# Performance work log

Hardware: AMD Instinct MI355X
Metric: run time of the kernel (lower is better)

## Reference

```python
import jax, jax.numpy as jnp
import numpy as np

D_MODEL, D_STATE, D_CONV, EXPAND = 1024, 16, 4, 2
D_INNER = EXPAND * D_MODEL          # 2048
DT_RANK = -(-D_MODEL // 16)        # 64
B_SZ, SEQ = 4, 2048


def setup_inputs() -> dict:
    key = jax.random.key(0)
    ks = jax.random.split(key, 10)
    s = 0.02
    x = jax.random.normal(ks[0], (B_SZ, SEQ, D_MODEL), jnp.float32)
    in_proj_w = s * jax.random.normal(ks[1], (2, 2 * D_INNER, D_MODEL), jnp.float32)
    conv_w = s * jax.random.normal(ks[2], (2, D_INNER, D_CONV), jnp.float32)
    conv_b = s * jax.random.normal(ks[3], (2, D_INNER), jnp.float32)
    x_proj_w = s * jax.random.normal(ks[4], (2, DT_RANK + 2 * D_STATE, D_INNER), jnp.float32)
    dt_proj_w = s * jax.random.normal(ks[5], (2, D_INNER, DT_RANK), jnp.float32)
    # bias chosen so softplus(dt) is small and the scan is stable (mamba-style dt init)
    dt_proj_b = jax.random.uniform(ks[6], (2, D_INNER), jnp.float32, -5.0, -3.0)
    # A_log = log(A) with A in [1, d_state], per real Mamba init (S4D-real)
    A_log = jnp.log(jax.random.uniform(ks[7], (2, D_INNER, D_STATE), jnp.float32, 1.0, float(D_STATE)))
    D_param = jnp.ones((2, D_INNER), jnp.float32) + s * jax.random.normal(ks[8], (2, D_INNER), jnp.float32)
    out_proj_w = s * jax.random.normal(ks[9], (2, D_MODEL, D_INNER), jnp.float32)
    return {"x": x, "in_proj_w": in_proj_w, "conv_w": conv_w, "conv_b": conv_b,
            "x_proj_w": x_proj_w, "dt_proj_w": dt_proj_w, "dt_proj_b": dt_proj_b,
            "A_log": A_log, "D_param": D_param, "out_proj_w": out_proj_w}


def _mamba(x, in_w, cw, cb, xw, dtw, dtb, A_log, Dp, ow):
    """Single-direction Mamba forward. x: [B, L, d_model]."""
    B, L, _ = x.shape
    xz = jnp.einsum('bld,ed->ble', x, in_w)          # [B, L, 2*d_inner]
    xi, z = jnp.split(xz, 2, axis=-1)
    # depthwise causal conv1d over time, kernel d_conv
    xp = jnp.pad(xi, ((0, 0), (D_CONV - 1, 0), (0, 0)))
    xc = cb + sum(cw[:, k] * xp[:, k:k + L, :] for k in range(D_CONV))
    xc = jax.nn.silu(xc)                              # [B, L, d_inner]
    proj = jnp.einsum('bld,ed->ble', xc, xw)          # [B, L, dt_rank+2*d_state]
    dt_raw, Bm, Cm = jnp.split(proj, [DT_RANK, DT_RANK + D_STATE], axis=-1)
    dt = jax.nn.softplus(jnp.einsum('blr,dr->bld', dt_raw, dtw) + dtb)  # [B, L, d_inner]
    A = -jnp.exp(A_log)                               # [d_inner, d_state]

    def step(h, inp):
        dt_t, B_t, C_t, x_t = inp                     # [B,d_inner],[B,S],[B,S],[B,d_inner]
        dA = jnp.exp(dt_t[..., None] * A)             # [B, d_inner, d_state]
        h = h * dA + (dt_t * x_t)[..., None] * B_t[:, None, :]
        y = jnp.einsum('bds,bs->bd', h, C_t)
        return h, y

    h0 = jnp.zeros((B, D_INNER, D_STATE), x.dtype)
    inps = (dt.transpose(1, 0, 2), Bm.transpose(1, 0, 2),
            Cm.transpose(1, 0, 2), xc.transpose(1, 0, 2))
    _, ys = jax.lax.scan(step, h0, inps)              # ys: [L, B, d_inner]
    y = ys.transpose(1, 0, 2) + xc * Dp
    y = y * jax.nn.silu(z)
    return jnp.einsum('bld,md->blm', y, ow)           # [B, L, d_model]


def reference(x, in_proj_w, conv_w, conv_b, x_proj_w, dt_proj_w, dt_proj_b, A_log, D_param, out_proj_w):
    y_f = _mamba(x, in_proj_w[0], conv_w[0], conv_b[0], x_proj_w[0],
                 dt_proj_w[0], dt_proj_b[0], A_log[0], D_param[0], out_proj_w[0])
    xb = jnp.flip(x, axis=1)
    y_b = _mamba(xb, in_proj_w[1], conv_w[1], conv_b[1], x_proj_w[1],
                 dt_proj_w[1], dt_proj_b[1], A_log[1], D_param[1], out_proj_w[1])
    return y_f + jnp.flip(y_b, axis=1)
```

## Files before the change

kernel.cpp:

```cpp
#include <hip/hip_runtime.h>
#include <hip/hip_bf16.h>
#include <math.h>
#include <stdio.h>


using u16 = unsigned short;
using u32 = unsigned int;

typedef __bf16 bf16x8 __attribute__((ext_vector_type(8)));
typedef float  f32x4  __attribute__((ext_vector_type(4)));
typedef u32    u32x4  __attribute__((ext_vector_type(4)));
typedef u16    u16x4  __attribute__((ext_vector_type(4)));

#define DEVINL __device__ __forceinline__

DEVINL float b2f(u16 u) { union { u32 i; float f; } v; v.i = ((u32)u) << 16; return v.f; }
DEVINL u16 f2b(float f) {
  union { float f; u32 i; } v; v.f = f;
  u32 i = v.i;
  return (u16)((i + 0x7FFFu + ((i >> 16) & 1u)) >> 16);
}

#define L2E 1.4426950408889634f
#define LN2 0.6931471805599453f

DEVINL float fast_silu(float a) {
  const float e = __builtin_amdgcn_exp2f(-a * L2E);
  return a * __builtin_amdgcn_rcpf(1.f + e);
}
DEVINL float fast_softplus(float x) {
  if (x > 20.f) return x;
  return LN2 * __builtin_amdgcn_logf(1.f + __builtin_amdgcn_exp2f(x * L2E));
}

DEVINL void gl_lds16(const u16* g, u16* l) {
  __builtin_amdgcn_global_load_lds(
      (__attribute__((address_space(1))) void*)const_cast<u16*>(g),
      (__attribute__((address_space(3))) void*)l, 16, 0, 0);
}

#define BAR()   asm volatile("s_barrier" ::: "memory")
#define LGKM0() asm volatile("s_waitcnt lgkmcnt(0)" ::: "memory")
#define VM6()   asm volatile("s_waitcnt vmcnt(6)" ::: "memory")
#define VM0()   asm volatile("s_waitcnt vmcnt(0)" ::: "memory")
#define NOPS    ((void)0)

__global__ __launch_bounds__(512, 2) void k_gemm256(
    const u16* __restrict__ A, int lda, int flipA,
    const u16* __restrict__ Bw, int ldb,
    u16* __restrict__ C, int ldc, int K)
{
  extern __shared__ __align__(16) char lds[];

  const int tid  = threadIdx.x;
  const int lane = tid & 63;
  const int wid  = tid >> 6;

  const int mBase = blockIdx.x * 256;
  const int nBase = blockIdx.y * 256;

  const int rloc = lane >> 3;
  const int scol = ((lane & 7) ^ rloc) << 3;
  const u16* srcA[2][2];
  const u16* srcB[2][2];
#pragma unroll
  for (int h = 0; h < 2; ++h)
#pragma unroll
    for (int i = 0; i < 2; ++i) {
      int ra = mBase + h * 128 + wid * 16 + i * 8 + rloc;
      if (flipA) ra ^= 2047;
      const int rb = nBase + h * 128 + wid * 16 + i * 8 + rloc;
      srcA[h][i] = A  + (long long)ra * lda + scol;
      srcB[h][i] = Bw + (long long)rb * ldb + scol;
    }
  u16* const dA = (u16*)lds + wid * 1024;
  u16* const dB = (u16*)lds + 32768 + wid * 1024;

  const int lhi16 = (lane >> 4) * 16;
  const int swz   = (lane & 7) << 4;
  const int rdA   = ((wid >> 2) * 64 + (lane & 15)) * 128 + (lhi16 ^ swz);
  const int rdAx  = rdA ^ 64;
  const int rdB   = 65536 + ((wid & 3) * 32 + (lane & 15)) * 128 + (lhi16 ^ swz);
  const int rdBx  = rdB ^ 64;

  f32x4 acc[2][2][4][2];
#pragma unroll
  for (int a = 0; a < 2; ++a)
#pragma unroll
    for (int b = 0; b < 2; ++b)
#pragma unroll
      for (int c = 0; c < 4; ++c)
#pragma unroll
        for (int d = 0; d < 2; ++d) acc[a][b][c][d] = (f32x4){0.f, 0.f, 0.f, 0.f};

  bf16x8 af[4][2], bq0[2][2], bq1[2][2];

#define LDSV(off) (*(const bf16x8*)(lds + (off)))
#define READ_A(CB, QM) do {                                                    \
  _Pragma("unroll") for (int fm = 0; fm < 4; ++fm) {                           \
    af[fm][0] = LDSV((CB)*32768 + (QM)*16384 + fm*2048 + rdA);                 \
    af[fm][1] = LDSV((CB)*32768 + (QM)*16384 + fm*2048 + rdAx); }              \
} while (0)
#define READ_B(CB, QN, DST) do {                                               \
  _Pragma("unroll") for (int fn = 0; fn < 2; ++fn) {                           \
    DST[fn][0] = LDSV((CB)*32768 + (QN)*16384 + fn*2048 + rdB);                \
    DST[fn][1] = LDSV((CB)*32768 + (QN)*16384 + fn*2048 + rdBx); }             \
} while (0)
#define MMA(QM, QN, BFR) do {                                                  \
  __builtin_amdgcn_s_setprio(1);                                              \
  _Pragma("unroll") for (int fm = 0; fm < 4; ++fm)                             \
  _Pragma("unroll") for (int fn = 0; fn < 2; ++fn)                             \
  _Pragma("unroll") for (int kk = 0; kk < 2; ++kk)                             \
    acc[QM][QN][fm][fn] = __builtin_amdgcn_mfma_f32_16x16x32_bf16(             \
        af[fm][kk], BFR[fn][kk], acc[QM][QN][fm][fn], 0, 0, 0);                \
  __builtin_amdgcn_s_setprio(0);                                              \
} while (0)
#define STAGE_A(CB, H, KT) do {                                                \
  gl_lds16(srcA[H][0] + (KT)*64, dA + (CB)*16384 + (H)*8192);                  \
  gl_lds16(srcA[H][1] + (KT)*64, dA + (CB)*16384 + (H)*8192 + 512);            \
} while (0)
#define STAGE_B(CB, H, KT) do {                                                \
  gl_lds16(srcB[H][0] + (KT)*64, dB + (CB)*16384 + (H)*8192);                  \
  gl_lds16(srcB[H][1] + (KT)*64, dB + (CB)*16384 + (H)*8192 + 512);            \
} while (0)

#define KTILE(CB, S1, S2, S3, S4, VMW) do {                                    \
  READ_A(CB, 0); READ_B(CB, 0, bq0);                                           \
  S1;                                                                          \
  LGKM0(); MMA(0, 0, bq0); BAR();                                              \
  READ_B(CB, 1, bq1);                                                          \
  S2;                                                                          \
  LGKM0(); MMA(0, 1, bq1); BAR();                                              \
  READ_A(CB, 1);                                                               \
  S3;                                                                          \
  LGKM0(); MMA(1, 1, bq1); BAR();                                              \
  S4; VMW;                                                                     \
  MMA(1, 0, bq0); BAR();                                                       \
} while (0)

  STAGE_A(0, 0, 0); STAGE_B(0, 0, 0); STAGE_A(0, 1, 0); STAGE_B(0, 1, 0);
  STAGE_A(1, 0, 1); STAGE_B(1, 1, 1); STAGE_A(1, 1, 1);
  VM6();
  BAR();

  const int niter = K >> 7;
  for (int it = 0; it < niter - 1; ++it) {
    const int kt = 2 * it;
    KTILE(0,
          STAGE_B(1, 0, kt + 1),
          STAGE_A(0, 0, kt + 2),
          STAGE_B(0, 1, kt + 2),
          STAGE_A(0, 1, kt + 2),
          VM6());
    KTILE(1,
          STAGE_B(0, 0, kt + 2),
          STAGE_A(1, 0, kt + 3),
          STAGE_B(1, 1, kt + 3),
          STAGE_A(1, 1, kt + 3),
          VM6());
  }
  {
    const int kt = 2 * (niter - 1);
    KTILE(0, STAGE_B(1, 0, kt + 1), NOPS, NOPS, NOPS, VM0());
    KTILE(1, NOPS, NOPS, NOPS, NOPS, NOPS);
  }

  const int rq = (lane >> 4) << 2;
  const int cn = lane & 15;
  const long long mW = mBase + (wid >> 2) * 64;
  const int nW = nBase + (wid & 3) * 32;
#pragma unroll
  for (int qm = 0; qm < 2; ++qm)
#pragma unroll
    for (int qn = 0; qn < 2; ++qn)
#pragma unroll
      for (int fm = 0; fm < 4; ++fm)
#pragma unroll
        for (int fn = 0; fn < 2; ++fn)
#pragma unroll
          for (int r = 0; r < 4; ++r) {
            const long long m = mW + qm * 128 + fm * 16 + rq + r;
            const int n = nW + qn * 128 + fn * 16 + cn;
            C[m * ldc + n] = f2b(acc[qm][qn][fm][fn][r]);
          }
#undef LDSV
#undef READ_A
#undef READ_B
#undef MMA
#undef STAGE_A
#undef STAGE_B
#undef KTILE
}

template <int MODE>
__global__ __launch_bounds__(256) void k_gemm(
    const u16* __restrict__ A, int lda, int flipA,
    const u16* __restrict__ Bw, int ldb,
    void* __restrict__ Cout, int ldc, int K,
    float* __restrict__ f1, float* __restrict__ f2,
    float* __restrict__ out2)
{
  __shared__ __align__(16) u16 As[128 * 64];
  __shared__ __align__(16) u16 Bs[128 * 64];

  const int tid  = threadIdx.x;
  const int lane = tid & 63;
  const int wid  = tid >> 6;

  const int mBase = blockIdx.x * 128;
  const int nBase = blockIdx.y * 128;

  f32x4 acc[4][4];
#pragma unroll
  for (int i = 0; i < 4; ++i)
#pragma unroll
    for (int j = 0; j < 4; ++j) acc[i][j] = (f32x4){0.f, 0.f, 0.f, 0.f};

  const int wm = (wid & 1) * 64;
  const int wn = (wid >> 1) * 64;
  const int lrow = lane & 15;
  const int lk   = (lane >> 4) * 8;
  const int sr = tid >> 3;
  const int sc = (tid & 7) * 8;

  for (int k0 = 0; k0 < K; k0 += 64) {
#pragma unroll
    for (int i = 0; i < 4; ++i) {
      int ra = mBase + i * 32 + sr;
      if (flipA) ra ^= 2047;
      const int rb = nBase + i * 32 + sr;
      u16* la = &As[(i * 256 + wid * 64) * 8];
      u16* lb = &Bs[(i * 256 + wid * 64) * 8];
      gl_lds16(A  + (long long)ra * lda + (k0 + sc), la);
      gl_lds16(Bw + (long long)rb * ldb + (k0 + sc), lb);
    }
    __syncthreads();
#pragma unroll
    for (int kk = 0; kk < 64; kk += 32) {
      bf16x8 af[4], bfr[4];
#pragma unroll
      for (int f = 0; f < 4; ++f) {
        af[f]  = *(const bf16x8*)&As[(wm + f * 16 + lrow) * 64 + kk + lk];
        bfr[f] = *(const bf16x8*)&Bs[(wn + f * 16 + lrow) * 64 + kk + lk];
      }
#pragma unroll
      for (int fm = 0; fm < 4; ++fm)
#pragma unroll
        for (int fn = 0; fn < 4; ++fn)
          acc[fm][fn] = __builtin_amdgcn_mfma_f32_16x16x32_bf16(af[fm], bfr[fn], acc[fm][fn], 0, 0, 0);
    }
    __syncthreads();
  }

  const int rowq = (lane >> 4) * 4;
  const int coln = lane & 15;
#pragma unroll
  for (int fm = 0; fm < 4; ++fm) {
#pragma unroll
    for (int fn = 0; fn < 4; ++fn) {
#pragma unroll
      for (int r = 0; r < 4; ++r) {
        const long long m = mBase + wm + fm * 16 + rowq + r;
        const long long n = nBase + wn + fn * 16 + coln;
        const float v = acc[fm][fn][r];
        if constexpr (MODE == 0) {
          ((u16*)Cout)[m * ldc + n] = f2b(v);
        } else if constexpr (MODE == 1) {
          ((u16*)Cout)[m * ldc + n] = f2b(fast_softplus(v + f1[(int)n]));
        } else if constexpr (MODE == 2) {
          ((float*)Cout)[m * ldc + n] = v;
        } else if constexpr (MODE == 3) {
          const long long mf = m ^ 2047;
          out2[mf * ldc + n] = v + f2[mf * ldc + n];
        } else {
          if (n < 64)       ((u16*)Cout)[m * ldc + n] = f2b(v);
          else if (n < 80)  f1[m * 16 + (n - 64)] = v;
          else if (n < 96)  f2[m * 16 + (n - 80)] = v;
        }
      }
    }
  }
}

__global__ __launch_bounds__(256) void k_prep(
    const float* __restrict__ inw_d, u16* __restrict__ inwB,
    const float* __restrict__ xpw_d, u16* __restrict__ xw_pad,
    const float* __restrict__ dtw_d, u16* __restrict__ dtwB,
    const float* __restrict__ alog_d, float* __restrict__ A2,
    const float* __restrict__ cw_d, float* __restrict__ cwT)
{
  const int bx = blockIdx.x;
  const int tid = threadIdx.x;
  if (bx < 4096) {
    const int i = bx * 256 + tid;
    const f32x4 v = ((const f32x4*)inw_d)[i];
    u16x4 o = {f2b(v[0]), f2b(v[1]), f2b(v[2]), f2b(v[3])};
    ((u16x4*)inwB)[i] = o;
  } else if (bx < 5120) {
    const int idx = (bx - 4096) * 256 + tid;
    const int c = idx & 2047, r = idx >> 11;
    xw_pad[idx] = (r < 96) ? f2b(xpw_d[r * 2048 + c]) : (u16)0;
  } else if (bx < 5248) {
    const int i = (bx - 5120) * 256 + tid;
    const f32x4 v = ((const f32x4*)dtw_d)[i];
    u16x4 o = {f2b(v[0]), f2b(v[1]), f2b(v[2]), f2b(v[3])};
    ((u16x4*)dtwB)[i] = o;
  } else if (bx < 5376) {
    const int idx = (bx - 5248) * 256 + tid;
    A2[idx] = -expf(alog_d[idx]) * L2E;
  } else {
    const int idx = (bx - 5376) * 256 + tid;
    const int d = idx & 2047, k = idx >> 11;
    cwT[k * 2048 + d] = cw_d[d * 4 + k];
  }
}

__global__ __launch_bounds__(256) void k_castw(const float* __restrict__ src,
                                               u16* __restrict__ dst) {
  const int i = blockIdx.x * 256 + threadIdx.x;
  const f32x4 v = ((const f32x4*)src)[i];
  u16x4 o = {f2b(v[0]), f2b(v[1]), f2b(v[2]), f2b(v[3])};
  ((u16x4*)dst)[i] = o;
}

__global__ __launch_bounds__(256) void k_cast_x(const float* __restrict__ x,
                                                u16* __restrict__ xA) {
  const int idx = blockIdx.x * 256 + threadIdx.x;
  const f32x4 v = ((const f32x4*)x)[idx];
  u16x4 o = {f2b(v[0]), f2b(v[1]), f2b(v[2]), f2b(v[3])};
  ((u16x4*)xA)[idx] = o;
}

__global__ __launch_bounds__(256) void k_conv(const u16* __restrict__ xz,
                                              const float* __restrict__ cwT,
                                              const float* __restrict__ cb,
                                              u16* __restrict__ xc) {
  const int idx = blockIdx.x * 256 + threadIdx.x;
  const int d8  = idx & 255;
  const int gr  = idx >> 8;
  const int t   = gr & 2047;
  const int d0  = d8 * 8;

  float acc[8];
  {
    const f32x4 b0 = *(const f32x4*)(cb + d0);
    const f32x4 b1 = *(const f32x4*)(cb + d0 + 4);
#pragma unroll
    for (int j = 0; j < 4; ++j) { acc[j] = b0[j]; acc[4 + j] = b1[j]; }
  }

#pragma unroll
  for (int k = 0; k < 4; ++k) {
    const int tt = t - 3 + k;
    if (tt < 0) continue;
    const u32x4 v = *(const u32x4*)(xz + (long long)(gr + k - 3) * 4096 + d0);
    const u16* pv = (const u16*)&v;
    const f32x4 w0 = *(const f32x4*)(cwT + k * 2048 + d0);
    const f32x4 w1 = *(const f32x4*)(cwT + k * 2048 + d0 + 4);
#pragma unroll
    for (int j = 0; j < 4; ++j) {
      acc[j]     = fmaf(w0[j], b2f(pv[j]), acc[j]);
      acc[4 + j] = fmaf(w1[j], b2f(pv[4 + j]), acc[4 + j]);
    }
  }
  u16 o[8];
#pragma unroll
  for (int j = 0; j < 8; ++j) {
    o[j] = f2b(fast_silu(acc[j]));
  }
  *(u32x4*)(xc + (long long)gr * 2048 + d0) = *(const u32x4*)o;
}

__global__ __launch_bounds__(256) void k_scanA(
    const u16* __restrict__ dt, const u16* __restrict__ xc,
    const float* __restrict__ Bf, const float* __restrict__ A2,
    float* __restrict__ hbuf, float* __restrict__ sumdt)
{
  const int tid = threadIdx.x;
  const int bx  = blockIdx.x;
  const int d     = (bx & 7) * 256 + tid;
  const int chunk = (bx >> 3) & 31;
  const int b     = bx >> 8;

  float a2[16];
#pragma unroll
  for (int s = 0; s < 16; ++s) a2[s] = A2[d * 16 + s];

  float h[16];
#pragma unroll
  for (int s = 0; s < 16; ++s) h[s] = 0.f;
  float sdt = 0.f;

  const long long rowBase = (long long)b * 2048 + chunk * 64;
  for (int t0 = 0; t0 < 64; ++t0) {
    const long long gr = rowBase + t0;
    const float dtv = b2f(dt[gr * 2048 + d]);
    const float xcv = b2f(xc[gr * 2048 + d]);
    sdt += dtv;
    const float dtx = dtv * xcv;
    float Bv[16];
    *(f32x4*)&Bv[0]  = *(const f32x4*)(Bf + gr * 16);
    *(f32x4*)&Bv[4]  = *(const f32x4*)(Bf + gr * 16 + 4);
    *(f32x4*)&Bv[8]  = *(const f32x4*)(Bf + gr * 16 + 8);
    *(f32x4*)&Bv[12] = *(const f32x4*)(Bf + gr * 16 + 12);
#pragma unroll
    for (int s = 0; s < 16; ++s) {
      const float dA = __builtin_amdgcn_exp2f(a2[s] * dtv);
      h[s] = fmaf(h[s], dA, dtx * Bv[s]);
    }
  }
  const long long cbi = (long long)b * 32 + chunk;
#pragma unroll
  for (int s = 0; s < 16; ++s) hbuf[(cbi * 16 + s) * 2048 + d] = h[s];
  sumdt[cbi * 2048 + d] = sdt;
}

__global__ __launch_bounds__(256) void k_scanB(
    const float* __restrict__ A2, float* __restrict__ hbuf,
    const float* __restrict__ sumdt)
{
  const int tid = threadIdx.x;
  const int bx  = blockIdx.x;
  const int d   = (bx & 7) * 256 + tid;
  const int sg  = ((bx >> 3) & 1) * 8;
  const int b   = bx >> 4;

  float a2[8];
#pragma unroll
  for (int s = 0; s < 8; ++s) a2[s] = A2[d * 16 + sg + s];
  float h[8];
#pragma unroll
  for (int s = 0; s < 8; ++s) h[s] = 0.f;

  const long long base = (long long)b * 32;
  for (int c = 0; c < 32; ++c) {
    const long long cbi = base + c;
    const float sd = sumdt[cbi * 2048 + d];
#pragma unroll
    for (int s = 0; s < 8; ++s) {
      float* p = &hbuf[(cbi * 16 + sg + s) * 2048 + d];
      const float loc = *p;
      *p = h[s];
      const float P = __builtin_amdgcn_exp2f(a2[s] * sd);
      h[s] = fmaf(h[s], P, loc);
    }
  }
}

__global__ __launch_bounds__(256) void k_scanC(
    const u16* __restrict__ dt, const u16* __restrict__ xc,
    const float* __restrict__ Bf, const float* __restrict__ Cf,
    const float* __restrict__ A2, const float* __restrict__ hbuf,
    const float* __restrict__ Dp, u16* __restrict__ yz)
{
  const int tid = threadIdx.x;
  const int bx  = blockIdx.x;
  const int d     = (bx & 7) * 256 + tid;
  const int chunk = (bx >> 3) & 31;
  const int b     = bx >> 8;
  const float dp  = Dp[d];

  float a2[16];
#pragma unroll
  for (int s = 0; s < 16; ++s) a2[s] = A2[d * 16 + s];

  const long long cbi = (long long)b * 32 + chunk;
  float h[16];
#pragma unroll
  for (int s = 0; s < 16; ++s) h[s] = hbuf[(cbi * 16 + s) * 2048 + d];

  const long long rowBase = (long long)b * 2048 + chunk * 64;
  for (int t0 = 0; t0 < 64; ++t0) {
    const long long gr = rowBase + t0;
    const float dtv = b2f(dt[gr * 2048 + d]);
    const float xcv = b2f(xc[gr * 2048 + d]);
    const float dtx = dtv * xcv;
    float Bv[16], Cv[16];
    *(f32x4*)&Bv[0]  = *(const f32x4*)(Bf + gr * 16);
    *(f32x4*)&Bv[4]  = *(const f32x4*)(Bf + gr * 16 + 4);
    *(f32x4*)&Bv[8]  = *(const f32x4*)(Bf + gr * 16 + 8);
    *(f32x4*)&Bv[12] = *(const f32x4*)(Bf + gr * 16 + 12);
    *(f32x4*)&Cv[0]  = *(const f32x4*)(Cf + gr * 16);
    *(f32x4*)&Cv[4]  = *(const f32x4*)(Cf + gr * 16 + 4);
    *(f32x4*)&Cv[8]  = *(const f32x4*)(Cf + gr * 16 + 8);
    *(f32x4*)&Cv[12] = *(const f32x4*)(Cf + gr * 16 + 12);
    float y = 0.f;
#pragma unroll
    for (int s = 0; s < 16; ++s) {
      const float dA = __builtin_amdgcn_exp2f(a2[s] * dtv);
      h[s] = fmaf(h[s], dA, dtx * Bv[s]);
      y = fmaf(h[s], Cv[s], y);
    }
    const float z = b2f(yz[gr * 4096 + 2048 + d]);
    const float yv = (y + xcv * dp) * fast_silu(z);
    yz[gr * 4096 + d] = f2b(yv);
  }
}

extern "C" void kernel_launch(void* const* d_in, const int* in_sizes, int n_in,
                              void* d_out, int out_size, void* d_ws, size_t ws_size,
                              hipStream_t stream) {
  const float* x    = (const float*)d_in[0];
  const float* inw  = (const float*)d_in[1];
  const float* cw   = (const float*)d_in[2];
  const float* cb   = (const float*)d_in[3];
  const float* xpw  = (const float*)d_in[4];
  const float* dtw  = (const float*)d_in[5];
  const float* dtb  = (const float*)d_in[6];
  const float* alog = (const float*)d_in[7];
  const float* Dp   = (const float*)d_in[8];
  const float* ow   = (const float*)d_in[9];
  float* out = (float*)d_out;

  char* ws = (char*)d_ws;
  float* outacc = (float*)(ws + 0);
  u16*   xz_d   = (u16*)(ws + 33554432);
  u16*   xc_d   = (u16*)(ws + 100663296);
  u16*   inwB   = (u16*)(ws + 100663296);
  u16*   dt_d   = (u16*)(ws + 134217728);
  u16*   owB    = (u16*)(ws + 134217728);
  u16*   xA     = (u16*)(ws + 167772160);
  u16*   proj_d = (u16*)(ws + 184549376);
  u16*   xw_pad = (u16*)(ws + 185597952);
  float* A2     = (float*)(ws + 186122240);
  float* Bf     = (float*)(ws + 186253312);
  float* Cf     = (float*)(ws + 186777600);
  float* hbuf   = (float*)(ws + 187301888);
  float* sumdt  = (float*)(ws + 204079104);
  u16*   dtwB   = (u16*)(ws + 205127680);
  float* cwT    = (float*)(ws + 205389824);
  const size_t NEED = 205422592;

  (void)in_sizes; (void)n_in; (void)out_size;
  if (ws_size < NEED) {
    fprintf(stderr, "[BiMamba] ws_size=%zu < needed %zu — aborting launch\n", ws_size, NEED);
    return;
  }

  static bool attr_set = false;
  if (!attr_set) {
    (void)hipFuncSetAttribute((const void*)k_gemm256,
                              hipFuncAttributeMaxDynamicSharedMemorySize, 131072);
    attr_set = true;
  }

  k_cast_x<<<8192, 256, 0, stream>>>(x, xA);

  for (int dir = 0; dir < 2; ++dir) {
    const float* inw_d = inw + (long long)dir * 4096 * 1024;
    const float* cw_d  = cw  + dir * 2048 * 4;
    const float* cb_d  = cb  + dir * 2048;
    const float* xpw_d = xpw + dir * 96 * 2048;
    const float* dtw_d = dtw + dir * 2048 * 64;
    const float* dtb_d = dtb + dir * 2048;
    const float* al_d  = alog + dir * 2048 * 16;
    const float* Dp_d  = Dp  + dir * 2048;
    const float* ow_d  = ow  + (long long)dir * 1024 * 2048;

    k_prep<<<5408, 256, 0, stream>>>(inw_d, inwB, xpw_d, xw_pad,
                                     dtw_d, dtwB, al_d, A2, cw_d, cwT);

    k_gemm256<<<dim3(32, 16), 512, 131072, stream>>>(
        xA, 1024, dir, inwB, 1024, xz_d, 4096, 1024);

    k_conv<<<8192, 256, 0, stream>>>(xz_d, cwT, cb_d, xc_d);

    k_gemm<4><<<dim3(64, 1), 256, 0, stream>>>(
        xc_d, 2048, 0, xw_pad, 2048, proj_d, 64, 2048, Bf, Cf, nullptr);

    k_gemm<1><<<dim3(64, 16), 256, 0, stream>>>(
        proj_d, 64, 0, dtwB, 64, dt_d, 2048, 64,
        const_cast<float*>(dtb_d), nullptr, nullptr);

    k_scanA<<<1024, 256, 0, stream>>>(dt_d, xc_d, Bf, A2, hbuf, sumdt);
    k_scanB<<<64, 256, 0, stream>>>(A2, hbuf, sumdt);
    k_scanC<<<1024, 256, 0, stream>>>(dt_d, xc_d, Bf, Cf, A2, hbuf, Dp_d, xz_d);

    k_castw<<<2048, 256, 0, stream>>>(ow_d, owB);

    if (dir == 0) {
      k_gemm<2><<<dim3(64, 8), 256, 0, stream>>>(
          xz_d, 4096, 0, owB, 2048, outacc, 1024, 2048, nullptr, nullptr, nullptr);
    } else {
      k_gemm<3><<<dim3(64, 8), 256, 0, stream>>>(
          xz_d, 4096, 0, owB, 2048, nullptr, 1024, 2048,
          nullptr, outacc, out);
    }
  }
}
```

Measured before the change: 759.7 us.

## Restructure 256-tile GEMM k-loop to stage full tiles with one barrier

Reworks the k-loop schedule of the 256x256 bf16 GEMM. Each k-tile now issues all eight global-to-LDS loads for the next tile up front, then reads every A and B fragment into separate register sets. Partial lgkmcnt waits with scheduling barriers let MFMAs start as fragments arrive, and there is a single barrier per tile instead of four. The goal is less barrier stalling and better overlap of LDS reads with MFMA work. In exchange it uses more fragment registers and hardcodes the iteration count for K=1024. It also drops the barrier between the vmcnt wait and the LDS reads, which risks a race on data loaded by other waves.

```diff
diff --git a/kernel.cpp b/kernel.cpp
--- a/kernel.cpp
+++ b/kernel.cpp
@@ -39,11 +39,12 @@
       (__attribute__((address_space(3))) void*)l, 16, 0, 0);
 }
 
-#define BAR()   asm volatile("s_barrier" ::: "memory")
-#define LGKM0() asm volatile("s_waitcnt lgkmcnt(0)" ::: "memory")
-#define VM6()   asm volatile("s_waitcnt vmcnt(6)" ::: "memory")
-#define VM0()   asm volatile("s_waitcnt vmcnt(0)" ::: "memory")
-#define NOPS    ((void)0)
+#define BAR()    asm volatile("s_barrier" ::: "memory")
+#define LGKM(N)  asm volatile("s_waitcnt lgkmcnt(" #N ")" ::: "memory")
+#define VM8()    asm volatile("s_waitcnt vmcnt(8)" ::: "memory")
+#define VM0()    asm volatile("s_waitcnt vmcnt(0)" ::: "memory")
+#define SCHB()   __builtin_amdgcn_sched_barrier(0)
+#define NOPS     ((void)0)
 
 __global__ __launch_bounds__(512, 2) void k_gemm256(
     const u16* __restrict__ A, int lda, int flipA,
@@ -93,77 +94,63 @@
 #pragma unroll
         for (int d = 0; d < 2; ++d) acc[a][b][c][d] = (f32x4){0.f, 0.f, 0.f, 0.f};
 
-  bf16x8 af[4][2], bq0[2][2], bq1[2][2];
+  bf16x8 af0[4][2], af1[4][2], bq0[2][2], bq1[2][2];
 
 #define LDSV(off) (*(const bf16x8*)(lds + (off)))
-#define READ_A(CB, QM) do {                                                    \
+#define READ_A(CB, QM, DST) do {                                               \
   _Pragma("unroll") for (int fm = 0; fm < 4; ++fm) {                           \
-    af[fm][0] = LDSV((CB)*32768 + (QM)*16384 + fm*2048 + rdA);                 \
-    af[fm][1] = LDSV((CB)*32768 + (QM)*16384 + fm*2048 + rdAx); }              \
+    DST[fm][0] = LDSV((CB)*32768 + (QM)*16384 + fm*2048 + rdA);                \
+    DST[fm][1] = LDSV((CB)*32768 + (QM)*16384 + fm*2048 + rdAx); }             \
 } while (0)
 #define READ_B(CB, QN, DST) do {                                               \
   _Pragma("unroll") for (int fn = 0; fn < 2; ++fn) {                           \
     DST[fn][0] = LDSV((CB)*32768 + (QN)*16384 + fn*2048 + rdB);                \
     DST[fn][1] = LDSV((CB)*32768 + (QN)*16384 + fn*2048 + rdBx); }             \
 } while (0)
-#define MMA(QM, QN, BFR) do {                                                  \
+#define MMA(QM, QN, AF, BFR) do {                                              \
   __builtin_amdgcn_s_setprio(1);                                              \
   _Pragma("unroll") for (int fm = 0; fm < 4; ++fm)                             \
   _Pragma("unroll") for (int fn = 0; fn < 2; ++fn)                             \
   _Pragma("unroll") for (int kk = 0; kk < 2; ++kk)                             \
     acc[QM][QN][fm][fn] = __builtin_amdgcn_mfma_f32_16x16x32_bf16(             \
-        af[fm][kk], BFR[fn][kk], acc[QM][QN][fm][fn], 0, 0, 0);                \
+        AF[fm][kk], BFR[fn][kk], acc[QM][QN][fm][fn], 0, 0, 0);                \
   __builtin_amdgcn_s_setprio(0);                                              \
 } while (0)
-#define STAGE_A(CB, H, KT) do {                                                \
-  gl_lds16(srcA[H][0] + (KT)*64, dA + (CB)*16384 + (H)*8192);                  \
-  gl_lds16(srcA[H][1] + (KT)*64, dA + (CB)*16384 + (H)*8192 + 512);            \
+#define STAGE_ALL(CB, KT) do {                                                 \
+  gl_lds16(srcA[0][0] + (KT)*64, dA + (CB)*16384);                             \
+  gl_lds16(srcA[0][1] + (KT)*64, dA + (CB)*16384 + 512);                       \
+  gl_lds16(srcA[1][0] + (KT)*64, dA + (CB)*16384 + 8192);                      \
+  gl_lds16(srcA[1][1] + (KT)*64, dA + (CB)*16384 + 8192 + 512);                \
+  gl_lds16(srcB[0][0] + (KT)*64, dB + (CB)*16384);                             \
+  gl_lds16(srcB[0][1] + (KT)*64, dB + (CB)*16384 + 512);                       \
+  gl_lds16(srcB[1][0] + (KT)*64, dB + (CB)*16384 + 8192);                      \
+  gl_lds16(srcB[1][1] + (KT)*64, dB + (CB)*16384 + 8192 + 512);                \
 } while (0)
-#define STAGE_B(CB, H, KT) do {                                                \
-  gl_lds16(srcB[H][0] + (KT)*64, dB + (CB)*16384 + (H)*8192);                  \
-  gl_lds16(srcB[H][1] + (KT)*64, dB + (CB)*16384 + (H)*8192 + 512);            \
+
+#define KTILE2(CB, STG, VMW) do {                                              \
+  STG;                                                                         \
+  VMW;                                                                         \
+  READ_A(CB, 0, af0); READ_B(CB, 0, bq0); READ_B(CB, 1, bq1);                  \
+  READ_A(CB, 1, af1);                                                          \
+  LGKM(12); SCHB();                                                            \
+  MMA(0, 0, af0, bq0);                                                         \
+  LGKM(8); SCHB();                                                             \
+  MMA(0, 1, af0, bq1);                                                         \
+  LGKM(0); SCHB();                                                             \
+  MMA(1, 1, af1, bq1);                                                         \
+  MMA(1, 0, af1, bq0);                                                         \
+  BAR();                                                                       \
 } while (0)
 
-#define KTILE(CB, S1, S2, S3, S4, VMW) do {                                    \
-  READ_A(CB, 0); READ_B(CB, 0, bq0);                                           \
-  S1;                                                                          \
-  LGKM0(); MMA(0, 0, bq0); BAR();                                              \
-  READ_B(CB, 1, bq1);                                                          \
-  S2;                                                                          \
-  LGKM0(); MMA(0, 1, bq1); BAR();                                              \
-  READ_A(CB, 1);                                                               \
-  S3;                                                                          \
-  LGKM0(); MMA(1, 1, bq1); BAR();                                              \
-  S4; VMW;                                                                     \
-  MMA(1, 0, bq0); BAR();                                                       \
-} while (0)
-
-  STAGE_A(0, 0, 0); STAGE_B(0, 0, 0); STAGE_A(0, 1, 0); STAGE_B(0, 1, 0);
-  STAGE_A(1, 0, 1); STAGE_B(1, 1, 1); STAGE_A(1, 1, 1);
-  VM6();
-  BAR();
-
-  const int niter = K >> 7;
-  for (int it = 0; it < niter - 1; ++it) {
+  STAGE_ALL(0, 0);
+
+  for (int it = 0; it < 7; ++it) {
     const int kt = 2 * it;
-    KTILE(0,
-          STAGE_B(1, 0, kt + 1),
-          STAGE_A(0, 0, kt + 2),
-          STAGE_B(0, 1, kt + 2),
-          STAGE_A(0, 1, kt + 2),
-          VM6());
-    KTILE(1,
-          STAGE_B(0, 0, kt + 2),
-          STAGE_A(1, 0, kt + 3),
-          STAGE_B(1, 1, kt + 3),
-          STAGE_A(1, 1, kt + 3),
-          VM6());
-  }
-  {
-    const int kt = 2 * (niter - 1);
-    KTILE(0, STAGE_B(1, 0, kt + 1), NOPS, NOPS, NOPS, VM0());
-    KTILE(1, NOPS, NOPS, NOPS, NOPS, NOPS);
-  }
+    KTILE2(0, STAGE_ALL(1, kt + 1), VM8());
+    KTILE2(1, STAGE_ALL(0, kt + 2), VM8());
+  }
+  KTILE2(0, STAGE_ALL(1, 15), VM8());
+  KTILE2(1, NOPS, VM0());
 
   const int rq = (lane >> 4) << 2;
   const int cn = lane & 15;
@@ -187,9 +174,8 @@
 #undef READ_A
 #undef READ_B
 #undef MMA
-#undef STAGE_A
-#undef STAGE_B
-#undef KTILE
+#undef STAGE_ALL
+#undef KTILE2
 }
 
 template <int MODE>
```

New measurement: 864.7 us. +13.8%, slower.
